# Performance work log

Hardware: AMD Instinct MI355X
Metric: run time of the kernel (lower is better)

Reference implementation:

```python
import jax, jax.numpy as jnp
import numpy as np

TEMPERATURE = 0.07


def setup_inputs() -> dict:
    key = jax.random.key(0)
    k1, k2 = jax.random.split(key)
    B, D = 4096, 256
    x = jax.random.normal(k1, (B, D), dtype=jnp.float32)
    y = jax.random.normal(k2, (B, D), dtype=jnp.float32)
    # L2-normalize so dot products lie in [-1, 1] (realistic contrastive
    # embeddings; keeps exp(dot / 0.07) finite as the original code assumes).
    x = x / jnp.linalg.norm(x, axis=-1, keepdims=True)
    y = y / jnp.linalg.norm(y, axis=-1, keepdims=True)
    return {"x": x, "y": y}


def reference(x, y):
    # Faithful translation of the (quirky) original loop:
    # for each row i, neg_dot starts at zeros and is filled one j at a time;
    # at EVERY inner step k the code computes exp(neg_dot/T) over the full
    # vector (entries j>k are still 0 -> exp=1) and accumulates
    #   loss += -log(exp[i] / sum(exp)).
    # Vectorized:
    #   S[i,j] = x_i . y_j / T
    #   denom[i,k] = sum_{j<=k} exp(S[i,j]) + (B-1-k)    (zeros contribute e^0)
    #   numer log term: S[i,i] if k>=i else 0 -> contributes (B-i)*S[i,i]
    B = x.shape[0]
    S = jnp.einsum("id,jd->ij", x, y) / TEMPERATURE          # [B, B]
    cumE = jnp.cumsum(jnp.exp(S), axis=1)                     # [B, B]
    k = jnp.arange(B, dtype=S.dtype)
    denom = cumE + (B - 1.0 - k)[None, :]                     # [B, B]
    diag = jnp.diagonal(S)                                    # [B]
    n_hits = (B - jnp.arange(B)).astype(S.dtype)              # k >= i count
    loss = jnp.sum(jnp.log(denom)) - jnp.sum(n_hits * diag)
    return loss
```

## Files before the change

### kernel.cpp

```cpp
#include <hip/hip_runtime.h>

typedef __bf16  bf16x8 __attribute__((ext_vector_type(8)));
typedef short   s16x8  __attribute__((ext_vector_type(8)));
typedef float   f32x4  __attribute__((ext_vector_type(4)));
typedef unsigned short u16;
typedef u16     u16x4  __attribute__((ext_vector_type(4)));
typedef unsigned int u32;

#define B_SZ 4096
#define D_SZ 256

static constexpr float SCALE = (float)(1.4426950408889634 / 0.07);
static constexpr float LN2F  = 0.69314718055994531f;

__device__ __forceinline__ u16 f2bf(float f) {
  unsigned u = __float_as_uint(f);
  unsigned r = u + 0x7FFFu + ((u >> 16) & 1u);
  return (u16)(r >> 16);
}
__device__ __forceinline__ float bf2f(u16 h) {
  return __uint_as_float((u32)h << 16);
}

template<bool BF>
__device__ __forceinline__ bf16x8 ld8(const u16* pb, const float* pf) {
  if constexpr (BF) {
    return *(const bf16x8*)pb;
  } else {
    f32x4 a = *(const f32x4*)pf;
    f32x4 b = *(const f32x4*)(pf + 4);
    s16x8 s;
#pragma unroll
    for (int i = 0; i < 4; ++i) { s[i] = (short)f2bf(a[i]); s[i + 4] = (short)f2bf(b[i]); }
    return __builtin_bit_cast(bf16x8, s);
  }
}

__global__ __launch_bounds__(256) void cl_convert(const float* __restrict__ x,
                                                  const float* __restrict__ y,
                                                  u16* __restrict__ xb,
                                                  u16* __restrict__ yb) {
  const int idx = (int)(blockIdx.x * 256 + threadIdx.x) * 4;
  f32x4 vx = *(const f32x4*)(x + idx);
  f32x4 vy = *(const f32x4*)(y + idx);
  u16x4 sx, sy;
#pragma unroll
  for (int i = 0; i < 4; ++i) { sx[i] = f2bf(vx[i]); sy[i] = f2bf(vy[i]); }
  *(u16x4*)(xb + idx) = sx;
  *(u16x4*)(yb + idx) = sy;
}

__global__ __launch_bounds__(512, 2) void cl_gemm2(const u16* __restrict__ xb,
                                                   const u16* __restrict__ yb,
                                                   u16* __restrict__ Sl) {
  __shared__ u16 As[2][256 * 64];
  __shared__ u16 Bs[2][256 * 64];
  const int tid  = threadIdx.x;
  const int lane = tid & 63;
  const int wv   = tid >> 6;
  const int l15  = lane & 15;
  const int lg   = lane >> 4;
  const int wr   = wv >> 1;
  const int wc   = wv & 1;
  int bid = (int)blockIdx.x;
  bid = (bid & 7) * 32 + (bid >> 3);
  const int brow = (bid >> 4) << 8;
  const int bcol = (bid & 15) << 8;

  const int rsub = (wv << 3) + (lane >> 3);
  const u32 cs0  = (u32)(((lane & 7) << 4) ^ ((lane >> 3) << 4));
  const char* aBase = (const char*)xb + ((size_t)(brow + rsub) << 9) + cs0;
  const char* bBase = (const char*)yb + ((size_t)(bcol + rsub) << 9) + cs0;
  const u32 dstOff = (u32)((wv << 10) + lane * 16);

  auto stage = [&](u16* panel, const char* base, int kt) {
#pragma unroll
    for (int i = 0; i < 4; ++i) {
      const char* g = base + i * 32768 + (kt << 7);
      auto lp = (__attribute__((address_space(3))) u32*)
                  ((char*)panel + i * 8192 + dstOff);
      __builtin_amdgcn_global_load_lds(
          (const __attribute__((address_space(1))) u32*)g, lp, 16, 0, 0);
    }
  };

  const u32 rowOffA = (u32)((((wr << 6) + l15) << 7));
  const u32 rowOffB = (u32)((((wc << 7) + l15) << 7));
  u32 colk[2];
#pragma unroll
  for (int ks = 0; ks < 2; ++ks)
    colk[ks] = (u32)(((ks << 6) + (lg << 4)) ^ ((l15 & 7) << 4));

  f32x4 acc[4][8] = {};

  stage(As[0], aBase, 0);
  stage(Bs[0], bBase, 0);
  __syncthreads();

#pragma unroll 1
  for (int kt = 0; kt < 4; ++kt) {
    if (kt < 3) {
      stage(As[(kt + 1) & 1], aBase, kt + 1);
      stage(Bs[(kt + 1) & 1], bBase, kt + 1);
    }
    const char* Ap = (const char*)As[kt & 1];
    const char* Bp = (const char*)Bs[kt & 1];
#pragma unroll
    for (int ks = 0; ks < 2; ++ks) {
      bf16x8 Af[4], Bf[8];
      const char* ap = Ap + rowOffA + colk[ks];
      const char* bp = Bp + rowOffB + colk[ks];
#pragma unroll
      for (int mi = 0; mi < 4; ++mi) Af[mi] = *(const bf16x8*)(ap + mi * 2048);
#pragma unroll
      for (int ni = 0; ni < 8; ++ni) Bf[ni] = *(const bf16x8*)(bp + ni * 2048);
#pragma unroll
      for (int mi = 0; mi < 4; ++mi)
#pragma unroll
        for (int ni = 0; ni < 8; ++ni)
          acc[mi][ni] = __builtin_amdgcn_mfma_f32_16x16x32_bf16(
              Bf[ni], Af[mi], acc[mi][ni], 0, 0, 0);
    }
    __syncthreads();
  }

#pragma unroll
  for (int mi = 0; mi < 4; ++mi)
#pragma unroll
    for (int ni = 0; ni < 8; ++ni) {
      u16x4 o;
#pragma unroll
      for (int v = 0; v < 4; ++v) o[v] = f2bf(acc[mi][ni][v] * SCALE);
      const int rs = brow + (wr << 6) + (mi << 4) + l15;
      const int cs = bcol + (wc << 7) + (ni << 4) + (lg << 2);
      *(u16x4*)(Sl + (size_t)rs * B_SZ + cs) = o;
    }
}

__global__ __launch_bounds__(256) void cl_scan(const u16* __restrict__ Sl,
                                               float* __restrict__ partials) {
  __shared__ float wtot[4];
  __shared__ float red2[4];
  const int row  = (int)blockIdx.x;
  const int tid  = threadIdx.x;
  const int lane = tid & 63;
  const int wv   = tid >> 6;

  const u16* rp = Sl + (size_t)row * B_SZ + tid * 16;
  s16x8 a = *(const s16x8*)rp;
  s16x8 b = *(const s16x8*)(rp + 8);
  float t[16], p[16];
  float run = 0.f;
#pragma unroll
  for (int j = 0; j < 8; ++j) { t[j] = bf2f((u16)a[j]); t[8 + j] = bf2f((u16)b[j]); }
#pragma unroll
  for (int j = 0; j < 16; ++j) { run += __builtin_amdgcn_exp2f(t[j]); p[j] = run; }

  float s = run;
#pragma unroll
  for (int d = 1; d < 64; d <<= 1) {
    float u = __shfl_up(s, (unsigned)d, 64);
    if (lane >= d) s += u;
  }
  if (lane == 63) wtot[wv] = s;
  __syncthreads();
  float off = 0.f;
#pragma unroll
  for (int w = 0; w < 4; ++w) if (w < wv) off += wtot[w];
  const float excl = off + (s - run);

  float lacc = 0.f;
  const int c0 = tid * 16;
#pragma unroll
  for (int j = 0; j < 16; ++j)
    lacc += __builtin_amdgcn_logf(excl + p[j] + (float)(B_SZ - 1 - (c0 + j)));
  if ((row >> 4) == tid) lacc -= (float)(B_SZ - row) * t[row & 15];
  lacc *= LN2F;

#pragma unroll
  for (int d = 1; d < 64; d <<= 1) lacc += __shfl_xor(lacc, d, 64);
  if (lane == 0) red2[wv] = lacc;
  __syncthreads();
  if (tid == 0)
    partials[row] = (red2[0] + red2[1]) + (red2[2] + red2[3]);
}

__global__ __launch_bounds__(256) void cl_final(const float* __restrict__ p,
                                                float* __restrict__ out) {
  __shared__ float red[256];
  const int tid = threadIdx.x;
  float s = 0.f;
#pragma unroll
  for (int k = 0; k < 16; ++k) s += p[tid + 256 * k];
  red[tid] = s;
  __syncthreads();
#pragma unroll
  for (int o = 128; o > 0; o >>= 1) {
    if (tid < o) red[tid] += red[tid + o];
    __syncthreads();
  }
  if (tid == 0) out[0] = red[0];
}

template<bool BF>
__global__ __launch_bounds__(256) void cl_main(const float* __restrict__ x,
                                               const float* __restrict__ y,
                                               const u16* __restrict__ xb,
                                               const u16* __restrict__ yb,
                                               float* __restrict__ partials) {
  __shared__ float st[16][68];
  __shared__ float red[256];
  const int tid  = threadIdx.x;
  const int lane = tid & 63;
  const int wv   = tid >> 6;
  const int l15  = lane & 15;
  const int lg   = lane >> 4;
  const int i0   = blockIdx.x * 16;

  bf16x8 A[8];
  {
    const size_t base = (size_t)(i0 + l15) * D_SZ + (lg << 3);
#pragma unroll
    for (int ks = 0; ks < 8; ++ks)
      A[ks] = ld8<BF>(xb + base + ks * 32, x + base + ks * 32);
  }

  float lacc = 0.f, carry = 0.f;

  auto load_b = [&](bf16x8 (&F)[8], int t) {
    const size_t jb = (size_t)(t * 64 + (wv << 4) + l15) * D_SZ + (lg << 3);
#pragma unroll
    for (int ks = 0; ks < 8; ++ks)
      F[ks] = ld8<BF>(yb + jb + ks * 32, y + jb + ks * 32);
  };

  auto body = [&](bf16x8 (&F)[8], int t) {
    f32x4 acc = {0.f, 0.f, 0.f, 0.f};
#pragma unroll
    for (int ks = 0; ks < 8; ++ks)
      acc = __builtin_amdgcn_mfma_f32_16x16x32_bf16(A[ks], F[ks], acc, 0, 0, 0);
    __syncthreads();
    const int colg = t * 64 + (wv << 4) + l15;
#pragma unroll
    for (int v = 0; v < 4; ++v) {
      float tv = acc[v] * SCALE;
      const int rowl = (lg << 2) + v;
      if (i0 + rowl == colg) lacc -= (float)(B_SZ - colg) * tv;
      st[rowl][(wv << 4) + l15] = tv;
    }
    __syncthreads();
    const int row = (wv << 2) + lg;
    f32x4 tv4 = *(const f32x4*)&st[row][l15 << 2];
    float e0 = __builtin_amdgcn_exp2f(tv4[0]);
    float e1 = __builtin_amdgcn_exp2f(tv4[1]);
    float e2 = __builtin_amdgcn_exp2f(tv4[2]);
    float e3 = __builtin_amdgcn_exp2f(tv4[3]);
    float p1 = e0 + e1, p2 = p1 + e2, p3 = p2 + e3;
    float s = p3;
#pragma unroll
    for (int d = 1; d < 16; d <<= 1) {
      float u = __shfl_up(s, (unsigned)d, 16);
      if (l15 >= d) s += u;
    }
    const float base = carry + (s - p3);
    const float c0 = (float)(B_SZ - 1 - (t * 64 + (l15 << 2)));
    lacc += __builtin_amdgcn_logf(base + e0 + c0)
          + __builtin_amdgcn_logf(base + p1 + (c0 - 1.f))
          + __builtin_amdgcn_logf(base + p2 + (c0 - 2.f))
          + __builtin_amdgcn_logf(base + p3 + (c0 - 3.f));
    carry += __shfl(s, 15, 16);
  };

  bf16x8 B0[8], B1[8];
  load_b(B0, 0);
#pragma unroll 1
  for (int t2 = 0; t2 < 32; ++t2) {
    const int t0 = t2 * 2;
    load_b(B1, t0 + 1);
    body(B0, t0);
    if (t0 + 2 < 64) load_b(B0, t0 + 2);
    body(B1, t0 + 1);
  }

  red[tid] = lacc * LN2F;
  __syncthreads();
#pragma unroll
  for (int o = 128; o > 0; o >>= 1) {
    if (tid < o) red[tid] += red[tid + o];
    __syncthreads();
  }
  if (tid == 0) partials[blockIdx.x] = red[0];
}

__global__ __launch_bounds__(256) void cl_reduce(const float* __restrict__ p,
                                                 float* __restrict__ out) {
  __shared__ float red[256];
  const int tid = threadIdx.x;
  red[tid] = p[tid];
  __syncthreads();
#pragma unroll
  for (int o = 128; o > 0; o >>= 1) {
    if (tid < o) red[tid] += red[tid + o];
    __syncthreads();
  }
  if (tid == 0) out[0] = red[0];
}

extern "C" void kernel_launch(void* const* d_in, const int* in_sizes, int n_in,
                              void* d_out, int out_size, void* d_ws, size_t ws_size,
                              hipStream_t stream) {
  const float* x = (const float*)d_in[0];
  const float* y = (const float*)d_in[1];
  float* out = (float*)d_out;
  const size_t BD = (size_t)B_SZ * D_SZ;

  float* partials = (float*)d_ws;
  u16* xb = (u16*)((char*)d_ws + 16384 + 256);
  u16* yb = xb + BD;
  u16* Sl = yb + BD;
  const size_t need = 16384 + 256 + 4 * BD + 2 * (size_t)B_SZ * B_SZ;

  if (ws_size >= need) {
    cl_convert<<<(int)(BD / 1024), 256, 0, stream>>>(x, y, xb, yb);
    cl_gemm2<<<256, 512, 0, stream>>>(xb, yb, Sl);
    cl_scan<<<B_SZ, 256, 0, stream>>>(Sl, partials);
    cl_final<<<1, 256, 0, stream>>>(partials, out);
  } else {
    float* fpart = (float*)d_ws;
    u16* fxb = (u16*)((char*)d_ws + 4096);
    u16* fyb = fxb + BD;
    const size_t fneed = 4096 + 4 * BD;
    if (ws_size >= fneed) {
      cl_convert<<<(int)(BD / 1024), 256, 0, stream>>>(x, y, fxb, fyb);
      cl_main<true><<<B_SZ / 16, 256, 0, stream>>>(x, y, fxb, fyb, fpart);
    } else {
      cl_main<false><<<B_SZ / 16, 256, 0, stream>>>(x, y, fxb, fyb, fpart);
    }
    cl_reduce<<<1, 256, 0, stream>>>(fpart, out);
  }
}
```

Measured before the change: 40.57 us.

## Load GEMM fragments directly from global into registers, dropping LDS staging

The bf16 GEMM kernel no longer stages A/B tiles through LDS with global_load_lds and barriers. Each wave now loads its MFMA fragments straight from global memory into registers, double-buffered in software across eight k-steps. This removes LDS traffic and __syncthreads, at the cost of more global/L2 reads (fragments are reused across waves only through cache) and higher register pressure. The scan kernel's diagonal extraction is also rewritten to index the per-thread register array by compile-time j, avoiding dynamic indexing.

```diff
diff --git a/kernel.cpp b/kernel.cpp
--- a/kernel.cpp
+++ b/kernel.cpp
@@ -50,11 +50,9 @@
   *(u16x4*)(yb + idx) = sy;
 }
 
-__global__ __launch_bounds__(512, 2) void cl_gemm2(const u16* __restrict__ xb,
+__global__ __launch_bounds__(512, 2) void cl_gemm3(const u16* __restrict__ xb,
                                                    const u16* __restrict__ yb,
                                                    u16* __restrict__ Sl) {
-  __shared__ u16 As[2][256 * 64];
-  __shared__ u16 Bs[2][256 * 64];
   const int tid  = threadIdx.x;
   const int lane = tid & 63;
   const int wv   = tid >> 6;
@@ -67,62 +65,46 @@
   const int brow = (bid >> 4) << 8;
   const int bcol = (bid & 15) << 8;
 
-  const int rsub = (wv << 3) + (lane >> 3);
-  const u32 cs0  = (u32)(((lane & 7) << 4) ^ ((lane >> 3) << 4));
-  const char* aBase = (const char*)xb + ((size_t)(brow + rsub) << 9) + cs0;
-  const char* bBase = (const char*)yb + ((size_t)(bcol + rsub) << 9) + cs0;
-  const u32 dstOff = (u32)((wv << 10) + lane * 16);
-
-  auto stage = [&](u16* panel, const char* base, int kt) {
-#pragma unroll
-    for (int i = 0; i < 4; ++i) {
-      const char* g = base + i * 32768 + (kt << 7);
-      auto lp = (__attribute__((address_space(3))) u32*)
-                  ((char*)panel + i * 8192 + dstOff);
-      __builtin_amdgcn_global_load_lds(
-          (const __attribute__((address_space(1))) u32*)g, lp, 16, 0, 0);
-    }
-  };
-
-  const u32 rowOffA = (u32)((((wr << 6) + l15) << 7));
-  const u32 rowOffB = (u32)((((wc << 7) + l15) << 7));
-  u32 colk[2];
-#pragma unroll
-  for (int ks = 0; ks < 2; ++ks)
-    colk[ks] = (u32)(((ks << 6) + (lg << 4)) ^ ((l15 & 7) << 4));
+  const char* aBase = (const char*)xb
+      + ((size_t)(brow + (wr << 6) + l15) << 9) + (lg << 4);
+  const char* bBase = (const char*)yb
+      + ((size_t)(bcol + (wc << 7) + l15) << 9) + (lg << 4);
 
   f32x4 acc[4][8] = {};
-
-  stage(As[0], aBase, 0);
-  stage(Bs[0], bBase, 0);
-  __syncthreads();
-
-#pragma unroll 1
-  for (int kt = 0; kt < 4; ++kt) {
-    if (kt < 3) {
-      stage(As[(kt + 1) & 1], aBase, kt + 1);
-      stage(Bs[(kt + 1) & 1], bBase, kt + 1);
-    }
-    const char* Ap = (const char*)As[kt & 1];
-    const char* Bp = (const char*)Bs[kt & 1];
-#pragma unroll
-    for (int ks = 0; ks < 2; ++ks) {
-      bf16x8 Af[4], Bf[8];
-      const char* ap = Ap + rowOffA + colk[ks];
-      const char* bp = Bp + rowOffB + colk[ks];
-#pragma unroll
-      for (int mi = 0; mi < 4; ++mi) Af[mi] = *(const bf16x8*)(ap + mi * 2048);
-#pragma unroll
-      for (int ni = 0; ni < 8; ++ni) Bf[ni] = *(const bf16x8*)(bp + ni * 2048);
-#pragma unroll
-      for (int mi = 0; mi < 4; ++mi)
-#pragma unroll
-        for (int ni = 0; ni < 8; ++ni)
-          acc[mi][ni] = __builtin_amdgcn_mfma_f32_16x16x32_bf16(
-              Bf[ni], Af[mi], acc[mi][ni], 0, 0, 0);
-    }
-    __syncthreads();
-  }
+  bf16x8 A0[4], B0[8], A1[4], B1[8];
+
+#define LOADF(Adst, Bdst, KS)                                                  \
+  do {                                                                         \
+    _Pragma("unroll")                                                          \
+    for (int mi = 0; mi < 4; ++mi)                                             \
+      Adst[mi] = *(const bf16x8*)(aBase + mi * 8192 + (KS) * 64);              \
+    _Pragma("unroll")                                                          \
+    for (int ni = 0; ni < 8; ++ni)                                             \
+      Bdst[ni] = *(const bf16x8*)(bBase + ni * 8192 + (KS) * 64);              \
+  } while (0)
+
+#define MMSTEP(Asrc, Bsrc)                                                     \
+  do {                                                                         \
+    _Pragma("unroll")                                                          \
+    for (int mi = 0; mi < 4; ++mi)                                             \
+      _Pragma("unroll")                                                        \
+      for (int ni = 0; ni < 8; ++ni)                                           \
+        acc[mi][ni] = __builtin_amdgcn_mfma_f32_16x16x32_bf16(                 \
+            Bsrc[ni], Asrc[mi], acc[mi][ni], 0, 0, 0);                         \
+  } while (0)
+
+  LOADF(A0, B0, 0);
+  LOADF(A1, B1, 1);
+  MMSTEP(A0, B0); LOADF(A0, B0, 2);
+  MMSTEP(A1, B1); LOADF(A1, B1, 3);
+  MMSTEP(A0, B0); LOADF(A0, B0, 4);
+  MMSTEP(A1, B1); LOADF(A1, B1, 5);
+  MMSTEP(A0, B0); LOADF(A0, B0, 6);
+  MMSTEP(A1, B1); LOADF(A1, B1, 7);
+  MMSTEP(A0, B0);
+  MMSTEP(A1, B1);
+#undef LOADF
+#undef MMSTEP
 
 #pragma unroll
   for (int mi = 0; mi < 4; ++mi)
@@ -174,7 +156,9 @@
 #pragma unroll
   for (int j = 0; j < 16; ++j)
     lacc += __builtin_amdgcn_logf(excl + p[j] + (float)(B_SZ - 1 - (c0 + j)));
-  if ((row >> 4) == tid) lacc -= (float)(B_SZ - row) * t[row & 15];
+#pragma unroll
+  for (int j = 0; j < 16; ++j)
+    if (row == c0 + j) lacc -= (float)(B_SZ - row) * t[j];
   lacc *= LN2F;
 
 #pragma unroll
@@ -322,7 +306,7 @@
 
   if (ws_size >= need) {
     cl_convert<<<(int)(BD / 1024), 256, 0, stream>>>(x, y, xb, yb);
-    cl_gemm2<<<256, 512, 0, stream>>>(xb, yb, Sl);
+    cl_gemm3<<<256, 512, 0, stream>>>(xb, yb, Sl);
     cl_scan<<<B_SZ, 256, 0, stream>>>(Sl, partials);
     cl_final<<<1, 256, 0, stream>>>(partials, out);
   } else {
```

New measurement: 56.69 us. 1.4x slower.
